# Kernel tuning notes

Measured on AMD Instinct MI355X. Metric: run time of the kernel, lower is better.

The kernel has to match this reference:

```python
import jax, jax.numpy as jnp
import numpy as np

N_STREAMS = 4096


def setup_inputs() -> dict:
    key = jax.random.key(0)
    # Plain Gaussian (well-separated singular values; the polar factor math is
    # identical to the module's eye + 0.01*randn init, just a different point).
    H_raw = jax.random.normal(key, (N_STREAMS, N_STREAMS), dtype=jnp.float32)
    return {"H_raw": H_raw}


def reference(H_raw) -> jnp.ndarray:
    # OrthogonalMixing.forward: orthogonal polar factor of H_raw via thin SVD.
    U, s, Vh = jnp.linalg.svd(H_raw, full_matrices=False)
    return U @ Vh  # (s, s), satisfies H^T H = I
```

## Files before the change

kernel.cpp:

```cpp
#include <hip/hip_runtime.h>
#include <hip/hip_bf16.h>
#include <hip/hip_fp16.h>

#define NN 4096
#define NGROW 8
#define NPOL 2
#define NITER (NGROW + NPOL)
#define NPOW 12
#define NTRI 528
#define PRESCALE 32.0f

using f16 = _Float16;
typedef __attribute__((ext_vector_type(4))) float f32x4;
typedef __attribute__((ext_vector_type(8))) f16 h16x8;

__device__ inline void gl_lds16(const void* g, void* l) {
  __builtin_amdgcn_global_load_lds(
      (const __attribute__((address_space(1))) unsigned int*)(unsigned long long)(uintptr_t)g,
      (__attribute__((address_space(3))) unsigned int*)(uintptr_t)l,
      16, 0, 0);
}

template <int EPI, int TRI>
__global__ __launch_bounds__(256, 4) void gemm_nt(
    const f16* __restrict__ P, const f16* __restrict__ Q,
    void* __restrict__ Out, const f16* __restrict__ aux,
    float alpha, float beta) {
  int bi, bj;
  if (TRI) {
    const int t = blockIdx.x;
    int r = (int)((sqrtf(8.0f * (float)t + 1.0f) - 1.0f) * 0.5f);
    while ((r + 1) * (r + 2) / 2 <= t) ++r;
    while (r * (r + 1) / 2 > t) --r;
    bi = r;
    bj = t - r * (r + 1) / 2;
  } else {
    bi = blockIdx.x;
    bj = blockIdx.y;
  }

  __shared__ f16 lp[128 * 64];
  __shared__ f16 lq[128 * 64];

  const int tid = threadIdx.x;
  const int lane = tid & 63;
  const int wv = tid >> 6;
  const int wr = wv >> 1, wc = wv & 1;

  const int m = lane & 15;
  const int qd = lane >> 4;
  const int lrow = lane >> 3;
  const int lchunk = lane & 7;

  f32x4 acc[4][4] = {};

  for (int k0 = 0; k0 < NN; k0 += 64) {
    __syncthreads();
#pragma unroll
    for (int s = 0; s < 4; ++s) {
      const int t = wv * 4 + s;
      const int r = t * 8 + lrow;
      const int gc = lchunk ^ (r & 7);
      const f16* gp = P + (size_t)(bi * 128 + r) * NN + k0 + gc * 8;
      gl_lds16(gp, &lp[t * 512 + lane * 8]);
      const f16* gq = Q + (size_t)(bj * 128 + r) * NN + k0 + gc * 8;
      gl_lds16(gq, &lq[t * 512 + lane * 8]);
    }
    __syncthreads();

#pragma unroll
    for (int sub = 0; sub < 2; ++sub) {
      h16x8 av[4], bv[4];
#pragma unroll
      for (int f = 0; f < 4; ++f) {
        const int ra = wr * 64 + f * 16 + m;
        const int ca = (sub * 4 + qd) ^ (ra & 7);
        av[f] = *(const h16x8*)&lp[ra * 64 + ca * 8];
        const int rb = wc * 64 + f * 16 + m;
        const int cb = (sub * 4 + qd) ^ (rb & 7);
        bv[f] = *(const h16x8*)&lq[rb * 64 + cb * 8];
      }
#pragma unroll
      for (int fr = 0; fr < 4; ++fr)
#pragma unroll
        for (int fc = 0; fc < 4; ++fc)
          acc[fr][fc] = __builtin_amdgcn_mfma_f32_16x16x32_f16(
              av[fr], bv[fc], acc[fr][fc], 0, 0, 0);
    }
  }

#pragma unroll
  for (int fr = 0; fr < 4; ++fr) {
#pragma unroll
    for (int fc = 0; fc < 4; ++fc) {
#pragma unroll
      for (int rg = 0; rg < 4; ++rg) {
        const int lr = wr * 64 + fr * 16 + qd * 4 + rg;
        const int lc = wc * 64 + fc * 16 + m;
        const size_t idx = (size_t)(bi * 128 + lr) * NN + bj * 128 + lc;
        float v = beta * acc[fr][fc][rg];
        if (alpha != 0.0f) v += alpha * (float)aux[idx];
        if (EPI == 0)
          ((f16*)Out)[idx] = (f16)v;
        else
          ((float*)Out)[idx] = v;
        if (TRI && bi != bj) {
          const size_t idxT = (size_t)(bj * 128 + lc) * NN + bi * 128 + lr;
          ((f16*)Out)[idxT] = (f16)v;
        }
      }
    }
  }
}

__global__ void transpose_h(const unsigned short* __restrict__ in,
                            unsigned short* __restrict__ out) {
  __shared__ unsigned short tile[64][65];
  const int tx = threadIdx.x & 63;
  const int ty = threadIdx.x >> 6;
  const int bx = blockIdx.x, by = blockIdx.y;
#pragma unroll
  for (int rr = 0; rr < 16; ++rr) {
    const int row = rr * 4 + ty;
    tile[row][tx] = in[(size_t)(by * 64 + row) * NN + bx * 64 + tx];
  }
  __syncthreads();
#pragma unroll
  for (int rr = 0; rr < 16; ++rr) {
    const int row = rr * 4 + ty;
    out[(size_t)(bx * 64 + row) * NN + by * 64 + tx] = tile[tx][row];
  }
}

__global__ __launch_bounds__(256) void powmv(const f16* __restrict__ A,
                                             const float* __restrict__ vin,
                                             const float* __restrict__ snin,
                                             float* __restrict__ vout,
                                             float* __restrict__ snout) {
  const float scale = rsqrtf(*snin);
  const int row = blockIdx.x * 4 + (threadIdx.x >> 6);
  const int lane = threadIdx.x & 63;
  const f16* arow = A + (size_t)row * NN;
  float acc = 0.0f;
#pragma unroll
  for (int p = 0; p < 8; ++p) {
    const int c = p * 512 + lane * 8;
    const h16x8 av = *(const h16x8*)(arow + c);
    const float4 w0 = *(const float4*)(vin + c);
    const float4 w1 = *(const float4*)(vin + c + 4);
    acc += (float)av[0] * w0.x + (float)av[1] * w0.y + (float)av[2] * w0.z +
           (float)av[3] * w0.w + (float)av[4] * w1.x + (float)av[5] * w1.y +
           (float)av[6] * w1.z + (float)av[7] * w1.w;
  }
  for (int off = 32; off; off >>= 1) acc += __shfl_down(acc, off, 64);
  if (lane == 0) {
    const float u = acc * scale;
    vout[row] = u;
    atomicAdd(snout, u * u);
  }
}

__global__ void init_pw(float* __restrict__ v0, float* __restrict__ slots) {
  const int t = threadIdx.x;
  if (t < 64) slots[t] = (t == 1) ? 1.0f : 0.0f;
  for (int i = t; i < NN; i += 256) {
    const unsigned h = (unsigned)i * 2654435761u;
    v0[i] = ((h >> 16) & 1) ? 0.015625f : -0.015625f;
  }
}

__global__ void reduce_sumsq(const float* __restrict__ h, float* __restrict__ slots) {
  float acc = 0.0f;
  const size_t total = (size_t)NN * NN;
  for (size_t i = (size_t)blockIdx.x * blockDim.x + threadIdx.x; i < total;
       i += (size_t)gridDim.x * blockDim.x) {
    const float v = h[i];
    acc += v * v;
  }
  for (int off = 32; off; off >>= 1) acc += __shfl_down(acc, off, 64);
  __shared__ float ws[4];
  const int lane = threadIdx.x & 63, wv = threadIdx.x >> 6;
  if (lane == 0) ws[wv] = acc;
  __syncthreads();
  if (threadIdx.x == 0) atomicAdd(&slots[0], ws[0] + ws[1] + ws[2] + ws[3]);
}

__global__ void scale_cast(const float* __restrict__ h, const float* __restrict__ slots,
                           f16* __restrict__ xb, int mode) {
  float inv = rsqrtf(slots[0]) * PRESCALE;
  if (mode) inv *= rsqrtf(1.10f * sqrtf(slots[1 + NPOW]));
  const size_t i = ((size_t)blockIdx.x * blockDim.x + threadIdx.x) * 4;
  const float4 v = *(const float4*)(h + i);
  union { f16 hh[4]; ushort4 u; } cvt;
  cvt.hh[0] = (f16)(v.x * inv);
  cvt.hh[1] = (f16)(v.y * inv);
  cvt.hh[2] = (f16)(v.z * inv);
  cvt.hh[3] = (f16)(v.w * inv);
  *(ushort4*)(xb + i) = cvt.u;
}

__global__ void rescale_f16(f16* __restrict__ a, const float* __restrict__ slots) {
  const float cA = 1.0f / (1.10f * sqrtf(slots[1 + NPOW]));
  const size_t i = ((size_t)blockIdx.x * 256 + threadIdx.x) * 8;
  h16x8 v = *(h16x8*)(a + i);
  h16x8 o;
#pragma unroll
  for (int j = 0; j < 8; ++j) o[j] = (f16)((float)v[j] * cA);
  *(h16x8*)(a + i) = o;
}

extern "C" void kernel_launch(void* const* d_in, const int* in_sizes, int n_in,
                              void* d_out, int out_size, void* d_ws, size_t ws_size,
                              hipStream_t stream) {
  (void)in_sizes; (void)n_in; (void)out_size; (void)ws_size;
  const float* H = (const float*)d_in[0];
  float* out = (float*)d_out;
  char* ws = (char*)d_ws;

  f16* P0 = (f16*)ws;
  f16* P1 = (f16*)(ws + ((size_t)32 << 20));
  f16* Ab = (f16*)(ws + ((size_t)64 << 20));
  f16* Bb = (f16*)((char*)d_out + ((size_t)32 << 20));
  float* v0 = (float*)d_out;
  float* v1 = (float*)((char*)d_out + 16384);
  float* slots = (float*)((char*)d_out + 32768);

  const dim3 gfull(32, 32), tb(256), gt(64, 64);

  init_pw<<<1, 256, 0, stream>>>(v0, slots);
  reduce_sumsq<<<1024, 256, 0, stream>>>(H, slots);
  scale_cast<<<(NN * (size_t)NN) / 4 / 256, 256, 0, stream>>>(H, slots, P0, 0);
  transpose_h<<<gt, tb, 0, stream>>>((const unsigned short*)P0, (unsigned short*)P1);
  gemm_nt<0, 1><<<NTRI, tb, 0, stream>>>(P1, P1, Ab, (f16*)nullptr, 0.0f, 1.0f);
  for (int k = 0; k < NPOW; ++k) {
    const float* vi = (k & 1) ? v1 : v0;
    float* vo = (k & 1) ? v0 : v1;
    powmv<<<1024, 256, 0, stream>>>(Ab, vi, &slots[1 + k], vo, &slots[2 + k]);
  }
  rescale_f16<<<(NN * (size_t)NN) / 8 / 256, 256, 0, stream>>>(Ab, slots);
  scale_cast<<<(NN * (size_t)NN) / 4 / 256, 256, 0, stream>>>(H, slots, P0, 1);

  f16* X = P0;
  f16* Y = P1;
  const float GA = 3.4445f, GB = -4.7750f, GC = 2.0315f;
  const float PA = 1.875f, PB = -1.25f, PC = 0.375f;

  for (int it = 0; it < NITER; ++it) {
    const bool polish = it >= NGROW;
    const bool last = (it == NITER - 1);
    const float qa = polish ? PA : GA, qb = polish ? PB : GB, qc = polish ? PC : GC;

    if (it > 0) {
      transpose_h<<<gt, tb, 0, stream>>>((const unsigned short*)X, (unsigned short*)Y);
      gemm_nt<0, 1><<<NTRI, tb, 0, stream>>>(Y, Y, Ab, (f16*)nullptr, 0.0f, 1.0f);
    }
    f16* Bdst = last ? Y : Bb;
    gemm_nt<0, 1><<<NTRI, tb, 0, stream>>>(Ab, Ab, Bdst, Ab, qb, qc);
    if (!last) {
      gemm_nt<0, 0><<<gfull, tb, 0, stream>>>(X, Bdst, Y, X, qa, 1.0f);
      f16* t = X; X = Y; Y = t;
    } else {
      gemm_nt<1, 0><<<gfull, tb, 0, stream>>>(X, Bdst, out, X, qa, 1.0f);
    }
  }
}
```

Baseline: 4.763 ms.

## Rewrite GEMM with 256x256 tiles, 8 waves, double-buffered LDS pipeline

Replaces the 128x128 single-buffered GEMM with a 256x256 tile kernel using 512 threads, double-buffered LDS, and interleaved global-to-LDS staging between MFMA quarter-steps with barriers and priority hints. Larger tiles raise arithmetic intensity and the pipeline is meant to hide load latency behind MFMAs. The triangular grid shrinks to 136 blocks and the full grid to 256, which risks underfilling the CUs. The 128KB of LDS per block also limits occupancy to one block per CU.

```diff
diff --git a/kernel.cpp b/kernel.cpp
--- a/kernel.cpp
+++ b/kernel.cpp
@@ -7,7 +7,8 @@
 #define NPOL 2
 #define NITER (NGROW + NPOL)
 #define NPOW 12
-#define NTRI 528
+#define NKT (NN / 64)
+#define NTRI 136
 #define PRESCALE 32.0f
 
 using f16 = _Float16;
@@ -22,7 +23,7 @@
 }
 
 template <int EPI, int TRI>
-__global__ __launch_bounds__(256, 4) void gemm_nt(
+__global__ __launch_bounds__(512, 2) void gemm_nt(
     const f16* __restrict__ P, const f16* __restrict__ Q,
     void* __restrict__ Out, const f16* __restrict__ aux,
     float alpha, float beta) {
@@ -39,65 +40,159 @@
     bj = blockIdx.y;
   }
 
-  __shared__ f16 lp[128 * 64];
-  __shared__ f16 lq[128 * 64];
+  __shared__ f16 lA[2][256 * 64];
+  __shared__ f16 lB[2][256 * 64];
 
   const int tid = threadIdx.x;
   const int lane = tid & 63;
   const int wv = tid >> 6;
-  const int wr = wv >> 1, wc = wv & 1;
-
+  const int wr = wv >> 2;
+  const int wc = wv & 3;
   const int m = lane & 15;
   const int qd = lane >> 4;
-  const int lrow = lane >> 3;
-  const int lchunk = lane & 7;
-
-  f32x4 acc[4][4] = {};
-
-  for (int k0 = 0; k0 < NN; k0 += 64) {
-    __syncthreads();
-#pragma unroll
-    for (int s = 0; s < 4; ++s) {
-      const int t = wv * 4 + s;
-      const int r = t * 8 + lrow;
-      const int gc = lchunk ^ (r & 7);
-      const f16* gp = P + (size_t)(bi * 128 + r) * NN + k0 + gc * 8;
-      gl_lds16(gp, &lp[t * 512 + lane * 8]);
-      const f16* gq = Q + (size_t)(bj * 128 + r) * NN + k0 + gc * 8;
-      gl_lds16(gq, &lq[t * 512 + lane * 8]);
-    }
-    __syncthreads();
-
-#pragma unroll
-    for (int sub = 0; sub < 2; ++sub) {
-      h16x8 av[4], bv[4];
-#pragma unroll
-      for (int f = 0; f < 4; ++f) {
-        const int ra = wr * 64 + f * 16 + m;
-        const int ca = (sub * 4 + qd) ^ (ra & 7);
-        av[f] = *(const h16x8*)&lp[ra * 64 + ca * 8];
-        const int rb = wc * 64 + f * 16 + m;
-        const int cb = (sub * 4 + qd) ^ (rb & 7);
-        bv[f] = *(const h16x8*)&lq[rb * 64 + cb * 8];
-      }
-#pragma unroll
-      for (int fr = 0; fr < 4; ++fr)
-#pragma unroll
-        for (int fc = 0; fc < 4; ++fc)
-          acc[fr][fc] = __builtin_amdgcn_mfma_f32_16x16x32_f16(
-              av[fr], bv[fc], acc[fr][fc], 0, 0, 0);
-    }
-  }
-
-#pragma unroll
-  for (int fr = 0; fr < 4; ++fr) {
+  const int srow = tid >> 3;
+  const int schk = tid & 7;
+
+  f32x4 acc[8][4] = {};
+
+#define STAGE_A(u_, kk_, b_)                                                  \
+  do {                                                                        \
+    const int rr_ = (u_)*64 + srow;                                           \
+    gl_lds16(P + (size_t)(bi * 256 + rr_) * NN + (kk_) + ((schk ^ (srow & 7)) * 8), \
+             &lA[b_][(u_)*4096 + tid * 8]);                                   \
+  } while (0)
+#define STAGE_B(u_, kk_, b_)                                                  \
+  do {                                                                        \
+    const int rr_ = (u_)*64 + srow;                                           \
+    gl_lds16(Q + (size_t)(bj * 256 + rr_) * NN + (kk_) + ((schk ^ (srow & 7)) * 8), \
+             &lB[b_][(u_)*4096 + tid * 8]);                                   \
+  } while (0)
+
+#define READ_B_FR(b_)                                                         \
+  do {                                                                        \
+    _Pragma("unroll") for (int cf = 0; cf < 4; ++cf)                          \
+    _Pragma("unroll") for (int ks = 0; ks < 2; ++ks) {                        \
+      const int rb = wc * 64 + cf * 16 + m;                                   \
+      const int cb = (ks * 4 + qd) ^ (rb & 7);                                \
+      bv[cf][ks] = *(const h16x8*)&lB[b_][rb * 64 + cb * 8];                  \
+    }                                                                         \
+  } while (0)
+#define READ_A_FR(b_, q_)                                                     \
+  do {                                                                        \
+    _Pragma("unroll") for (int rf = 0; rf < 2; ++rf)                          \
+    _Pragma("unroll") for (int ks = 0; ks < 2; ++ks) {                        \
+      const int ra = wr * 128 + (q_)*32 + rf * 16 + m;                        \
+      const int ca = (ks * 4 + qd) ^ (ra & 7);                                \
+      av[rf][ks] = *(const h16x8*)&lA[b_][ra * 64 + ca * 8];                  \
+    }                                                                         \
+  } while (0)
+#define MFMA_Q(q_)                                                            \
+  do {                                                                        \
+    _Pragma("unroll") for (int rf = 0; rf < 2; ++rf)                          \
+    _Pragma("unroll") for (int cf = 0; cf < 4; ++cf)                          \
+    _Pragma("unroll") for (int ks = 0; ks < 2; ++ks)                          \
+        acc[(q_)*2 + rf][cf] = __builtin_amdgcn_mfma_f32_16x16x32_f16(        \
+            av[rf][ks], bv[cf][ks], acc[(q_)*2 + rf][cf], 0, 0, 0);           \
+  } while (0)
+
+#define BAR() __builtin_amdgcn_s_barrier()
+#define SCHEDB() __builtin_amdgcn_sched_barrier(0)
+#define PRIO(x_) __builtin_amdgcn_s_setprio(x_)
+#define VMCNT(n_) asm volatile("s_waitcnt vmcnt(" #n_ ")" ::: "memory")
+
+  STAGE_B(0, 0, 0); STAGE_B(1, 0, 0); STAGE_B(2, 0, 0); STAGE_B(3, 0, 0);
+  STAGE_A(0, 0, 0); STAGE_A(1, 0, 0); STAGE_A(2, 0, 0); STAGE_A(3, 0, 0);
+  STAGE_B(0, 64, 1); STAGE_B(1, 64, 1); STAGE_B(2, 64, 1); STAGE_B(3, 64, 1);
+  STAGE_A(0, 64, 1); STAGE_A(2, 64, 1);
+  VMCNT(6);
+  BAR();
+
+  for (int t = 0; t < NKT - 2; ++t) {
+    const int buf = t & 1, nbuf = buf ^ 1;
+    const int k1 = (t + 1) * 64, k2 = (t + 2) * 64;
+    h16x8 av[2][2], bv[4][2];
+    READ_B_FR(buf);
+    READ_A_FR(buf, 0);
+    STAGE_A(1, k1, nbuf); STAGE_A(3, k1, nbuf);
+    BAR(); SCHEDB();
+    PRIO(1); MFMA_Q(0); PRIO(0);
+    BAR();
+    READ_A_FR(buf, 1);
+    STAGE_B(0, k2, buf); STAGE_B(1, k2, buf);
+    BAR(); SCHEDB();
+    PRIO(1); MFMA_Q(1); PRIO(0);
+    VMCNT(10);
+    BAR();
+    READ_A_FR(buf, 2);
+    STAGE_B(2, k2, buf); STAGE_B(3, k2, buf);
+    BAR(); SCHEDB();
+    PRIO(1); MFMA_Q(2); PRIO(0);
+    BAR();
+    READ_A_FR(buf, 3);
+    STAGE_A(0, k2, buf); STAGE_A(2, k2, buf);
+    BAR(); SCHEDB();
+    PRIO(1); MFMA_Q(3); PRIO(0);
+    VMCNT(8);
+    BAR();
+  }
+
+  {
+    const int t = NKT - 2;
+    const int buf = t & 1, nbuf = buf ^ 1;
+    const int k1 = (t + 1) * 64;
+    h16x8 av[2][2], bv[4][2];
+    READ_B_FR(buf);
+    READ_A_FR(buf, 0);
+    STAGE_A(1, k1, nbuf); STAGE_A(3, k1, nbuf);
+    BAR(); SCHEDB();
+    PRIO(1); MFMA_Q(0); PRIO(0);
+    BAR();
+    READ_A_FR(buf, 1);
+    BAR(); SCHEDB();
+    PRIO(1); MFMA_Q(1); PRIO(0);
+    VMCNT(8);
+    BAR();
+    READ_A_FR(buf, 2);
+    BAR(); SCHEDB();
+    PRIO(1); MFMA_Q(2); PRIO(0);
+    BAR();
+    READ_A_FR(buf, 3);
+    BAR(); SCHEDB();
+    PRIO(1); MFMA_Q(3); PRIO(0);
+    VMCNT(2);
+    BAR();
+  }
+  {
+    const int buf = (NKT - 1) & 1;
+    h16x8 av[2][2], bv[4][2];
+    READ_B_FR(buf);
+    READ_A_FR(buf, 0);
+    BAR(); SCHEDB();
+    PRIO(1); MFMA_Q(0); PRIO(0);
+    BAR();
+    READ_A_FR(buf, 1);
+    BAR(); SCHEDB();
+    PRIO(1); MFMA_Q(1); PRIO(0);
+    VMCNT(0);
+    BAR();
+    READ_A_FR(buf, 2);
+    BAR(); SCHEDB();
+    PRIO(1); MFMA_Q(2); PRIO(0);
+    BAR();
+    READ_A_FR(buf, 3);
+    BAR(); SCHEDB();
+    PRIO(1); MFMA_Q(3); PRIO(0);
+  }
+
+#pragma unroll
+  for (int fr = 0; fr < 8; ++fr) {
 #pragma unroll
     for (int fc = 0; fc < 4; ++fc) {
 #pragma unroll
       for (int rg = 0; rg < 4; ++rg) {
-        const int lr = wr * 64 + fr * 16 + qd * 4 + rg;
+        const int lr = wr * 128 + fr * 16 + qd * 4 + rg;
         const int lc = wc * 64 + fc * 16 + m;
-        const size_t idx = (size_t)(bi * 128 + lr) * NN + bj * 128 + lc;
+        const size_t idx = (size_t)(bi * 256 + lr) * NN + bj * 256 + lc;
         float v = beta * acc[fr][fc][rg];
         if (alpha != 0.0f) v += alpha * (float)aux[idx];
         if (EPI == 0)
@@ -105,12 +200,21 @@
         else
           ((float*)Out)[idx] = v;
         if (TRI && bi != bj) {
-          const size_t idxT = (size_t)(bj * 128 + lc) * NN + bi * 128 + lr;
+          const size_t idxT = (size_t)(bj * 256 + lc) * NN + bi * 256 + lr;
           ((f16*)Out)[idxT] = (f16)v;
         }
       }
     }
   }
+#undef STAGE_A
+#undef STAGE_B
+#undef READ_B_FR
+#undef READ_A_FR
+#undef MFMA_Q
+#undef BAR
+#undef SCHEDB
+#undef PRIO
+#undef VMCNT
 }
 
 __global__ void transpose_h(const unsigned short* __restrict__ in,
@@ -225,13 +329,13 @@
   float* v1 = (float*)((char*)d_out + 16384);
   float* slots = (float*)((char*)d_out + 32768);
 
-  const dim3 gfull(32, 32), tb(256), gt(64, 64);
+  const dim3 gfull(16, 16), tbg(512), tb(256), gt(64, 64);
 
   init_pw<<<1, 256, 0, stream>>>(v0, slots);
   reduce_sumsq<<<1024, 256, 0, stream>>>(H, slots);
   scale_cast<<<(NN * (size_t)NN) / 4 / 256, 256, 0, stream>>>(H, slots, P0, 0);
   transpose_h<<<gt, tb, 0, stream>>>((const unsigned short*)P0, (unsigned short*)P1);
-  gemm_nt<0, 1><<<NTRI, tb, 0, stream>>>(P1, P1, Ab, (f16*)nullptr, 0.0f, 1.0f);
+  gemm_nt<0, 1><<<NTRI, tbg, 0, stream>>>(P1, P1, Ab, (f16*)nullptr, 0.0f, 1.0f);
   for (int k = 0; k < NPOW; ++k) {
     const float* vi = (k & 1) ? v1 : v0;
     float* vo = (k & 1) ? v0 : v1;
@@ -252,15 +356,15 @@
 
     if (it > 0) {
       transpose_h<<<gt, tb, 0, stream>>>((const unsigned short*)X, (unsigned short*)Y);
-      gemm_nt<0, 1><<<NTRI, tb, 0, stream>>>(Y, Y, Ab, (f16*)nullptr, 0.0f, 1.0f);
+      gemm_nt<0, 1><<<NTRI, tbg, 0, stream>>>(Y, Y, Ab, (f16*)nullptr, 0.0f, 1.0f);
     }
     f16* Bdst = last ? Y : Bb;
-    gemm_nt<0, 1><<<NTRI, tb, 0, stream>>>(Ab, Ab, Bdst, Ab, qb, qc);
+    gemm_nt<0, 1><<<NTRI, tbg, 0, stream>>>(Ab, Ab, Bdst, Ab, qb, qc);
     if (!last) {
-      gemm_nt<0, 0><<<gfull, tb, 0, stream>>>(X, Bdst, Y, X, qa, 1.0f);
+      gemm_nt<0, 0><<<gfull, tbg, 0, stream>>>(X, Bdst, Y, X, qa, 1.0f);
       f16* t = X; X = Y; Y = t;
     } else {
-      gemm_nt<1, 0><<<gfull, tb, 0, stream>>>(X, Bdst, out, X, qa, 1.0f);
+      gemm_nt<1, 0><<<gfull, tbg, 0, stream>>>(X, Bdst, out, X, qa, 1.0f);
     }
   }
 }
```

Result: no change. 4.769 ms (+0.1%).
